# Kernel tuning notes

Hardware: AMD Instinct MI355X
Metric: run time of the kernel (lower is better)

## Reference

```python
import jax, jax.numpy as jnp
import numpy as np

SR = 22050
L = 65537            # signal length; chosen so rfft length == L (required by source broadcast)
NFFT = 131072        # 2**ceil(log2(L))
RLEN = NFFT // 2 + 1 # == L
OUT_SIZE = 65537     # output_size init arg
BANDS = [("delta", 1.0, 4.0), ("theta", 4.0, 8.0), ("alpha", 8.0, 13.0),
         ("beta", 13.0, 30.0), ("gamma", 30.0, 100.0), ("high_gamma", 100.0, 200.0)]
SPEC = [("schumann", 7.83), ("healing", 528.0), ("solfeggio", 396.0), ("sleep", 2.5),
        ("focus", 14.1), ("harmony", 432.0), ("meditation", 6.0), ("energy", 30.0)]
FREQS_NP = np.fft.rfftfreq(NFFT, d=1.0 / SR).astype(np.float32)


def _prog_mean(hp, W1, b1, W2, b2, W3, b3):
    # vectorized get_harmonic_progression(arange(L)).mean()
    t = jnp.arange(L, dtype=jnp.float32)
    tn = (t / OUT_SIZE)[:, None]                       # [L,1]
    h = jax.nn.relu(tn @ W1 + b1)
    h = jax.nn.relu(h @ W2 + b2)
    mp = h @ W3 + b3                                   # [L,8]
    mod_depth = mp[0, 1]
    chord_idx = jnp.floor(t * 8.0 / OUT_SIZE).astype(jnp.int32) % 8
    chord = hp[chord_idx]                              # [L,4]
    chord = chord * (1.0 + mod_depth * jnp.sin(2.0 * jnp.pi * t / OUT_SIZE))[:, None]
    return chord.mean()


def _gain(bw, fw, hp, W1, b1, W2, b2, W3, b3):
    # all modulation is data-independent -> single [RLEN] multiplicative gain
    t = jnp.arange(L, dtype=jnp.float32)
    gain = jnp.ones(RLEN, dtype=jnp.float32)
    for k, (_, low, high) in enumerate(BANDS):
        center = (low + high) / 2.0
        width = (high - low) / 2.0
        m_np = np.exp(-0.5 * ((FREQS_NP - center) / (width / 2.0)) ** 2)
        m_np[(FREQS_NP < low) | (FREQS_NP > high)] = 0.0
        if not np.any(m_np > 0.01):  # static branch (mask is data-independent)
            continue
        mask = jnp.asarray(m_np.astype(np.float32))     # [RLEN] == [L]
        time_mod = jnp.sin(2.0 * jnp.pi * center * t / SR)
        gain = gain * (1.0 + mask * bw[k] * (1.0 + 0.2 * time_mod))
    pm = _prog_mean(hp, W1, b1, W2, b2, W3, b3)
    ws = min(15, NFFT // 100)
    ws = ws if ws > 0 else 1
    for j, (_, f) in enumerate(SPEC):
        if f >= SR / 2:
            continue
        for mult in (1.0, 2.0, 3.0, 4.0, 5.0):
            hf = f * mult
            if hf >= SR / 2:
                continue
            hidx = int(np.argmin(np.abs(FREQS_NP - hf)))
            s = max(0, hidx - ws)
            e = min(RLEN - 1, hidx + ws)
            if s >= e:
                continue
            idxs = np.arange(s, e + 1)
            win = jnp.asarray(np.exp(-0.5 * ((idxs - hidx) / (ws / 3.0)) ** 2).astype(np.float32))
            enh = fw[j] * win * (1.0 / mult ** 1.2) * (1.0 + pm)
            gain = gain.at[s:e + 1].multiply(1.0 + enh)
    return gain


def _forward(x, bw, fw, hp, W1, b1, W2, b2, W3, b3):
    gain = _gain(bw, fw, hp, W1, b1, W2, b2, W3, b3)    # [RLEN]
    xp = jnp.pad(x, ((0, 0), (0, 0), (0, NFFT - L)))    # zero-pad to n_fft
    X = jnp.fft.rfft(xp, axis=-1) * gain                # [B,C,RLEN] complex
    mag = jnp.abs(X)
    ph = jnp.angle(X)
    mid = 0.7 * mag[..., 1:-1] + 0.15 * mag[..., :-2] + 0.15 * mag[..., 2:]
    mag_s = jnp.concatenate([mag[..., :1], mid, mag[..., -1:]], axis=-1)
    Xc = mag_s * jnp.exp(1j * ph)
    y = jnp.fft.irfft(Xc, n=NFFT, axis=-1)[..., :L]
    return y.astype(x.dtype)


def setup_inputs() -> dict:
    key = jax.random.key(0)
    ks = jax.random.split(key, 8)
    B, C = 128, 2
    x = jax.random.normal(ks[0], (B, C, L), dtype=jnp.float32)
    band_weights = jnp.full((6,), 0.5, dtype=jnp.float32)
    freq_weights = jnp.full((8,), 0.3, dtype=jnp.float32)
    harmonic_progression = jax.random.normal(ks[1], (8, 4), dtype=jnp.float32)
    W1 = jax.random.normal(ks[2], (1, 32), dtype=jnp.float32)
    b1 = jnp.zeros((32,), dtype=jnp.float32)
    W2 = jax.random.normal(ks[3], (32, 16), dtype=jnp.float32) * (1.0 / np.sqrt(32.0))
    b2 = jnp.zeros((16,), dtype=jnp.float32)
    W3 = jax.random.normal(ks[4], (16, 8), dtype=jnp.float32) * (1.0 / np.sqrt(16.0))
    b3 = jnp.zeros((8,), dtype=jnp.float32)
    return {"x": x, "band_weights": band_weights, "freq_weights": freq_weights,
            "harmonic_progression": harmonic_progression,
            "W1": W1, "b1": b1, "W2": W2, "b2": b2, "W3": W3, "b3": b3}


def reference(x, band_weights, freq_weights, harmonic_progression, W1, b1, W2, b2, W3, b3):
    return _forward(x, band_weights, freq_weights, harmonic_progression, W1, b1, W2, b2, W3, b3)
```

## Files before the change

### kernel.cpp

```cpp
#include <hip/hip_runtime.h>
#include <hip/hip_fp16.h>
#include <math.h>

#define L_SIG 65537
#define NH    65536
#define NSIG  256
#define PI_F  3.14159265358979323846f

struct alignas(8) c32 { float x, y; };
typedef __half2 h2;
__device__ __forceinline__ c32 mkc(float a, float b){ c32 r; r.x=a; r.y=b; return r; }
__device__ __forceinline__ c32 cadd(c32 a, c32 b){ return mkc(a.x+b.x, a.y+b.y); }
__device__ __forceinline__ c32 csub(c32 a, c32 b){ return mkc(a.x-b.x, a.y-b.y); }
__device__ __forceinline__ c32 cmul(c32 a, c32 b){ return mkc(a.x*b.x - a.y*b.y, a.x*b.y + a.y*b.x); }
__device__ __forceinline__ h2  c2h(c32 a){ return __floats2half2_rn(a.x, a.y); }
__device__ __forceinline__ c32 h2c(h2 a){ float2 f = __half22float2(a); return mkc(f.x, f.y); }

template<int S>
__device__ __forceinline__ void fft16(c32 v[16]) {
  constexpr float C16[16] = {
    1.0f, 0.9238795325112867f, 0.7071067811865476f, 0.3826834323650898f,
    0.0f,-0.3826834323650898f,-0.7071067811865476f,-0.9238795325112867f,
   -1.0f,-0.9238795325112867f,-0.7071067811865476f,-0.3826834323650898f,
    0.0f, 0.3826834323650898f, 0.7071067811865476f, 0.9238795325112867f };
  constexpr float S16[16] = {
    0.0f, 0.3826834323650898f, 0.7071067811865476f, 0.9238795325112867f,
    1.0f, 0.9238795325112867f, 0.7071067811865476f, 0.3826834323650898f,
    0.0f,-0.3826834323650898f,-0.7071067811865476f,-0.9238795325112867f,
   -1.0f,-0.9238795325112867f,-0.7071067811865476f,-0.3826834323650898f };
  c32 s[16];
  #pragma unroll
  for (int b0 = 0; b0 < 4; ++b0) {
    c32 x0=v[b0], x1=v[b0+4], x2=v[b0+8], x3=v[b0+12];
    c32 u0=cadd(x0,x2), u1=csub(x0,x2), u2=cadd(x1,x3), u3=csub(x1,x3);
    c32 iu3 = mkc(-u3.y, u3.x);
    c32 yy[4];
    yy[0]=cadd(u0,u2); yy[2]=csub(u0,u2);
    if (S < 0) { yy[1]=csub(u1,iu3); yy[3]=cadd(u1,iu3); }
    else       { yy[1]=cadd(u1,iu3); yy[3]=csub(u1,iu3); }
    #pragma unroll
    for (int c0 = 0; c0 < 4; ++c0) {
      const int p = (b0*c0) & 15;
      c32 w = mkc(C16[p], (S<0) ? -S16[p] : S16[p]);
      s[c0*4 + b0] = cmul(yy[c0], w);
    }
  }
  #pragma unroll
  for (int c0 = 0; c0 < 4; ++c0) {
    c32 x0=s[c0*4+0], x1=s[c0*4+1], x2=s[c0*4+2], x3=s[c0*4+3];
    c32 u0=cadd(x0,x2), u1=csub(x0,x2), u2=cadd(x1,x3), u3=csub(x1,x3);
    c32 iu3 = mkc(-u3.y, u3.x);
    c32 yy[4];
    yy[0]=cadd(u0,u2); yy[2]=csub(u0,u2);
    if (S < 0) { yy[1]=csub(u1,iu3); yy[3]=cadd(u1,iu3); }
    else       { yy[1]=cadd(u1,iu3); yy[3]=csub(u1,iu3); }
    v[c0+0]=yy[0]; v[c0+4]=yy[1]; v[c0+8]=yy[2]; v[c0+12]=yy[3];
  }
}

template<int S>
__device__ __forceinline__ void fft256_team(c32 v[16], int r, int t, c32* sc) {
  fft16<S>(v);
  float ang = (float)S * (2.0f*PI_F/256.0f) * (float)r;
  c32 st; __sincosf(ang, &st.y, &st.x);
  c32 w = st;
  #pragma unroll
  for (int c = 1; c < 16; ++c) { v[c] = cmul(v[c], w); w = cmul(w, st); }
  int p  = r*8 + (t & 7);
  int fr = (r & 1) << 3;
  __syncthreads();
  if (t < 8) {
    #pragma unroll
    for (int c = 0; c < 16; ++c)
      sc[c*128 + (p ^ ((c & 1) << 3))] = v[c];
  }
  __syncthreads();
  if (t < 8) {
    #pragma unroll
    for (int a = 0; a < 16; ++a)
      v[a] = sc[r*128 + ((a*8 + (t & 7)) ^ fr)];
  }
  __syncthreads();
  if (t >= 8) {
    #pragma unroll
    for (int c = 0; c < 16; ++c)
      sc[c*128 + (p ^ ((c & 1) << 3))] = v[c];
  }
  __syncthreads();
  if (t >= 8) {
    #pragma unroll
    for (int a = 0; a < 16; ++a)
      v[a] = sc[r*128 + ((a*8 + (t & 7)) ^ fr)];
  }
  fft16<S>(v);
}

__global__ __launch_bounds__(256) void k_pm(const float* __restrict__ hp,
                                            float* __restrict__ pm_part) {
  __shared__ float r0[256], r1[256];
  int t = threadIdx.x, b = blockIdx.x;
  int gid = b*256 + t;
  float s0 = 0.f, s1 = 0.f;
  for (int tt = gid; tt < 65537; tt += 16384) {
    int ci = (tt * 8) / 65537;
    float cs = hp[ci*4+0] + hp[ci*4+1] + hp[ci*4+2] + hp[ci*4+3];
    float ang = (6.2831853071795864769f * (float)tt) / 65537.0f;
    s0 += cs;
    s1 += cs * sinf(ang);
  }
  r0[t] = s0; r1[t] = s1;
  __syncthreads();
  for (int s = 128; s > 0; s >>= 1) {
    if (t < s) { r0[t] += r0[t+s]; r1[t] += r1[t+s]; }
    __syncthreads();
  }
  if (t == 0) { pm_part[2*b] = r0[0]; pm_part[2*b+1] = r1[0]; }
}

__global__ __launch_bounds__(256) void k_prep2(const float* __restrict__ b1,
    const float* __restrict__ W2, const float* __restrict__ b2,
    const float* __restrict__ W3, const float* __restrict__ b3,
    const float* __restrict__ fw, const float* __restrict__ pm_part,
    float* __restrict__ pm_out, int* __restrict__ hidx, float* __restrict__ amp) {
  __shared__ float r0[64], r1[64];
  __shared__ float s_pm;
  int t = threadIdx.x;
  if (t < 64) { r0[t] = pm_part[2*t]; r1[t] = pm_part[2*t+1]; }
  __syncthreads();
  if (t == 0) {
    float h1[32], h2v[16];
    for (int i=0;i<32;i++){ float z = b1[i]; h1[i] = z > 0.f ? z : 0.f; }
    for (int o=0;o<16;o++){ float acc = b2[o];
      for (int i=0;i<32;i++) acc += h1[i]*W2[i*16+o];
      h2v[o] = acc > 0.f ? acc : 0.f; }
    float md = b3[1];
    for (int i=0;i<16;i++) md += h2v[i]*W3[i*8+1];
    float S0 = 0.f, S1 = 0.f;
    for (int i=0;i<64;i++){ S0 += r0[i]; S1 += r1[i]; }
    s_pm = (S0 + md*S1) / (65537.0f * 4.0f);
    pm_out[0] = s_pm;
  }
  __syncthreads();
  if (t < 40) {
    const double SPECF[8] = {7.83, 528.0, 396.0, 2.5, 14.1, 432.0, 6.0, 30.0};
    int j = t / 5, mi = t % 5;
    double mult = (double)(mi + 1);
    double hf = SPECF[j] * mult;
    double ratio = hf * (131072.0 / 22050.0);
    hidx[t] = (int)floor(ratio + 0.5);
    amp[t] = (float)((double)fw[j] * pow(mult, -1.2) * (1.0 + (double)s_pm));
  }
}

__global__ __launch_bounds__(256) void k_gain(float* __restrict__ gain,
    const float* __restrict__ bw, const int* __restrict__ hidx,
    const float* __restrict__ amp) {
  int i = blockIdx.x*256 + threadIdx.x;
  if (i >= 65537) return;
  float f = (float)((double)i * (22050.0/131072.0));
  float g = 1.0f;
  constexpr double LO[6] = {1,4,8,13,30,100};
  constexpr double HI[6] = {4,8,13,30,100,200};
  #pragma unroll
  for (int k = 0; k < 6; ++k) {
    float center = (float)(0.5*(LO[k]+HI[k]));
    float sig    = (float)(0.25*(HI[k]-LO[k]));
    float dm = (f - center)/sig;
    float mask = expf(-0.5f*dm*dm);
    if (f < (float)LO[k] || f > (float)HI[k]) mask = 0.f;
    float ang = (float)(6.283185307179586*0.5*(LO[k]+HI[k])) * (float)i / 22050.0f;
    g *= 1.0f + mask * bw[k] * (1.0f + 0.2f*sinf(ang));
  }
  for (int l = 0; l < 40; ++l) {
    int d = i - hidx[l];
    if (d >= -15 && d <= 15) {
      float dd = (float)d * 0.2f;
      g *= 1.0f + amp[l] * expf(-0.5f*dd*dd);
    }
  }
  gain[i] = g;
}

__global__ __launch_bounds__(256, 4) void k_fwd1(const float* __restrict__ x,
                                                 h2* __restrict__ A, int s0) {
  __shared__ float smem[4096];
  c32* sc = (c32*)smem;
  h2*  stg = (h2*)smem;
  int b = blockIdx.x; int sl = b >> 4; int g = b & 15;
  int t = threadIdx.x & 15, r = threadIdx.x >> 4;
  int n1 = g*16 + t;
  const float* xb = x + (size_t)(s0 + sl) * L_SIG;
  c32 v[16];
  #pragma unroll
  for (int j = 0; j < 16; ++j) {
    int n = n1 + 256*r + 4096*j;
    c32 z = mkc(0.f, 0.f);
    if (n < 32768)       { z.x = xb[2*n]; z.y = xb[2*n+1]; }
    else if (n == 32768) { z.x = xb[65536]; }
    v[j] = z;
  }
  fft256_team<-1>(v, r, t, sc);
  float a0 = -(2.0f*PI_F/65536.0f) * (float)(n1 * r);
  float a1 = -(2.0f*PI_F/4096.0f)  * (float)n1;
  c32 wb, wst;
  __sincosf(a0, &wb.y, &wb.x);
  __sincosf(a1, &wst.y, &wst.x);
  #pragma unroll
  for (int j = 0; j < 16; ++j) { v[j] = cmul(v[j], wb); wb = cmul(wb, wst); }
  __syncthreads();
  #pragma unroll
  for (int j = 0; j < 16; ++j)
    stg[(r + 16*j)*16 + t] = c2h(v[j]);
  __syncthreads();
  h2* Ab = A + (size_t)sl * NH;
  int u = threadIdx.x & 15, k2b = threadIdx.x >> 4;
  #pragma unroll
  for (int m = 0; m < 16; ++m) {
    int k2 = k2b + 16*m;
    Ab[(size_t)k2*256 + g*16 + u] = stg[k2*16 + u];
  }
}

__global__ __launch_bounds__(256, 4) void k_fwd2(const h2* __restrict__ A,
                                                 h2* __restrict__ B) {
  __shared__ float smem[4160];
  c32* sc = (c32*)smem;
  h2* stg = (h2*)smem;
  int b = blockIdx.x; int sl = b >> 4; int g = b & 15;
  int tid = threadIdx.x;
  int t = tid & 15, r = tid >> 4;
  const h2* Ab = A + (size_t)sl * NH;
  #pragma unroll
  for (int m = 0; m < 4; ++m) {
    int flat = tid + 256*m;
    int row = flat >> 6, i = flat & 63;
    float4 z = ((const float4*)(Ab + (size_t)(g*16 + row)*256))[i];
    *((float4*)&stg[row*260 + 4*i]) = z;
  }
  __syncthreads();
  c32 v[16];
  #pragma unroll
  for (int j = 0; j < 16; ++j)
    v[j] = h2c(stg[t*260 + r + 16*j]);
  fft256_team<-1>(v, r, t, sc);
  h2* Bb = B + (size_t)sl * NH;
  int k2 = g*16 + t;
  #pragma unroll
  for (int j = 0; j < 16; ++j) Bb[(size_t)k2 + 256*(r + 16*j)] = c2h(v[j]);
}

__global__ __launch_bounds__(256) void k_mid(const h2* __restrict__ Z,
    h2* __restrict__ Zc, const float* __restrict__ gain) {
  __shared__ c32 XL[258], XH[258];
  __shared__ float ML[258], MH[258];
  __shared__ float TC[258], TS[258];
  int b = blockIdx.x; int s = b >> 7; int blk = b & 127;
  int k0 = blk << 8;
  const h2* Zs = Z + (size_t)s * NH;
  h2* Os = Zc + (size_t)s * NH;
  int t = threadIdx.x;
  for (int e = t; e < 258; e += 256) {
    int k = k0 - 1 + e;
    bool kv = (k >= 0);
    int kc = kv ? k : 0;
    c32 zk = h2c(Zs[k & (NH-1)]);
    c32 zb = h2c(Zs[(NH - k) & (NH-1)]);
    c32 Aa = mkc(0.5f*(zk.x + zb.x), 0.5f*(zk.y - zb.y));
    c32 Bm = mkc(0.5f*(zk.x - zb.x), 0.5f*(zk.y + zb.y));
    float sn, cn; __sincosf((PI_F/65536.0f)*(float)k, &sn, &cn);
    TC[e] = cn; TS[e] = sn;
    c32 wB = cmul(mkc(-sn, -cn), Bm);
    float gk = gain[kc];
    float gK = gain[NH - kc];
    c32 Xk = mkc((Aa.x + wB.x)*gk,  (Aa.y + wB.y)*gk);
    c32 XK = mkc((Aa.x - wB.x)*gK, -(Aa.y - wB.y)*gK);
    float nk = Xk.x*Xk.x + Xk.y*Xk.y;
    float nK = XK.x*XK.x + XK.y*XK.y;
    float rk = rsqrtf(nk), rK = rsqrtf(nK);
    c32 Uk = (nk > 0.f) ? mkc(Xk.x*rk, Xk.y*rk) : mkc(1.f, 0.f);
    c32 UK = (nK > 0.f) ? mkc(XK.x*rK, XK.y*rK) : mkc(1.f, 0.f);
    float mk = (kv && nk > 0.f) ? nk*rk : 0.f;
    float mK = (kv && nK > 0.f) ? nK*rK : 0.f;
    XL[e] = Uk;  ML[e] = mk;
    XH[257-e] = UK; MH[257-e] = mK;
  }
  __syncthreads();
  {
    int q = t; int k = k0 + q;
    float m = ML[q+1];
    float msm = (k == 0) ? m : 0.7f*m + 0.15f*(ML[q] + ML[q+2]);
    c32 U = XL[q+1];
    c32 XcL = mkc(U.x*msm, U.y*msm);
    int K = NH - k;
    int eH = 256 - q;
    float mh = MH[eH];
    float msh = (K == 65536) ? mh : 0.7f*mh + 0.15f*(MH[eH-1] + MH[eH+1]);
    c32 Uh = XH[eH];
    c32 XcH = mkc(Uh.x*msh, Uh.y*msh);
    c32 E = mkc(0.5f*(XcL.x + XcH.x), 0.5f*(XcL.y - XcH.y));
    c32 D = mkc(0.5f*(XcL.x - XcH.x), 0.5f*(XcL.y + XcH.y));
    c32 O = cmul(mkc(TC[q+1], TS[q+1]), D);
    const float invN = 1.0f/65536.0f;
    Os[k] = c2h(mkc((E.x - O.y)*invN, (E.y + O.x)*invN));
    if (k != 0) Os[K] = c2h(mkc((E.x + O.y)*invN, (O.x - E.y)*invN));
  }
  if (blk == 127 && t == 0) {
    float m = ML[257];
    float msm = 0.7f*m + 0.15f*(ML[256] + MH[1]);
    c32 U = XL[257];
    const float invN = 1.0f/65536.0f;
    Os[32768] = c2h(mkc(U.x*msm*invN, -U.y*msm*invN));
  }
}

__global__ __launch_bounds__(256, 4) void k_inv1(const h2* __restrict__ Zc,
                                                 h2* __restrict__ B) {
  __shared__ float smem[4096];
  c32* sc = (c32*)smem;
  h2*  stg = (h2*)smem;
  int b = blockIdx.x;
  int idx = b >> 3;
  int sl = idx >> 1;
  int g = ((b & 7) << 1) | (idx & 1);
  int t = threadIdx.x & 15, r = threadIdx.x >> 4;
  int a = g*16 + t;
  const h2* Zs = Zc + (size_t)sl * NH;
  c32 v[16];
  #pragma unroll
  for (int j = 0; j < 16; ++j) v[j] = h2c(Zs[(size_t)a + 256*(r + 16*j)]);
  fft256_team<1>(v, r, t, sc);
  float a0 = (2.0f*PI_F/65536.0f) * (float)(a * r);
  float a1 = (2.0f*PI_F/4096.0f)  * (float)a;
  c32 wb, wst;
  __sincosf(a0, &wb.y, &wb.x);
  __sincosf(a1, &wst.y, &wst.x);
  #pragma unroll
  for (int j = 0; j < 16; ++j) { v[j] = cmul(v[j], wb); wb = cmul(wb, wst); }
  __syncthreads();
  #pragma unroll
  for (int j = 0; j < 16; ++j)
    stg[(r + 16*j)*16 + t] = c2h(v[j]);
  __syncthreads();
  h2* Bb = B + (size_t)sl * NH;
  int u = threadIdx.x & 15, m2b = threadIdx.x >> 4;
  #pragma unroll
  for (int m = 0; m < 16; ++m) {
    int m2 = m2b + 16*m;
    Bb[(size_t)m2*256 + g*16 + u] = stg[m2*16 + u];
  }
}

__global__ __launch_bounds__(256, 4) void k_inv2(const h2* __restrict__ B,
                                                 float* __restrict__ out, int s0) {
  __shared__ float smem[4160];
  c32* sc = (c32*)smem;
  h2* stg = (h2*)smem;
  int b = blockIdx.x; int sl = b >> 4; int g = b & 15;
  int tid = threadIdx.x;
  int t = tid & 15, r = tid >> 4;
  const h2* Bb = B + (size_t)sl * NH;
  #pragma unroll
  for (int m = 0; m < 4; ++m) {
    int flat = tid + 256*m;
    int row = flat >> 6, i = flat & 63;
    float4 z = ((const float4*)(Bb + (size_t)(g*16 + row)*256))[i];
    *((float4*)&stg[row*260 + 4*i]) = z;
  }
  __syncthreads();
  c32 v[16];
  #pragma unroll
  for (int j = 0; j < 16; ++j)
    v[j] = h2c(stg[t*260 + r + 16*j]);
  fft256_team<1>(v, r, t, sc);
  float* yb = out + (size_t)(s0 + sl) * L_SIG;
  int m2 = g*16 + t;
  #pragma unroll
  for (int j = 0; j < 16; ++j) {
    int m1 = r + 16*j;
    if (m1 <= 127) {
      int m = m2 + 256*m1;
      yb[2*m]   = v[j].x;
      yb[2*m+1] = v[j].y;
    } else if (m1 == 128 && m2 == 0) {
      yb[65536] = v[j].x;
    }
  }
}

extern "C" void kernel_launch(void* const* d_in, const int* in_sizes, int n_in,
                              void* d_out, int out_size, void* d_ws, size_t ws_size,
                              hipStream_t stream) {
  const float* x  = (const float*)d_in[0];
  const float* bw = (const float*)d_in[1];
  const float* fw = (const float*)d_in[2];
  const float* hp = (const float*)d_in[3];
  const float* b1 = (const float*)d_in[5];
  const float* W2 = (const float*)d_in[6];
  const float* b2 = (const float*)d_in[7];
  const float* W3 = (const float*)d_in[8];
  const float* b3 = (const float*)d_in[9];
  float* out = (float*)d_out;
  char* ws = (char*)d_ws;

  const size_t perSig = (size_t)NH * sizeof(h2);
  const size_t tail   = (size_t)L_SIG * sizeof(float) + 2048;
  size_t cap = (ws_size > tail) ? (ws_size - tail) / (2*perSig) : 1;
  int chunk = (cap >= (size_t)NSIG) ? NSIG : (cap < 1 ? 1 : (int)cap);

  h2*    A    = (h2*)ws;
  h2*    Bb   = (h2*)(ws + (size_t)chunk*perSig);
  float* gain = (float*)(ws + 2*(size_t)chunk*perSig);
  float* pm   = gain + L_SIG;
  int*   hidx = (int*)(pm + 1);
  float* amp  = (float*)(hidx + 40);
  float* pm_part = amp + 40;

  k_pm   <<<64, 256, 0, stream>>>(hp, pm_part);
  k_prep2<<<1,  256, 0, stream>>>(b1, W2, b2, W3, b3, fw, pm_part, pm, hidx, amp);
  k_gain <<<257,256, 0, stream>>>(gain, bw, hidx, amp);

  for (int s0 = 0; s0 < NSIG; s0 += chunk) {
    int S = (NSIG - s0 < chunk) ? (NSIG - s0) : chunk;
    k_fwd1<<<S*16, 256, 0, stream>>>(x, A, s0);
    k_fwd2<<<S*16, 256, 0, stream>>>(A, Bb);
    k_mid <<<S*128,256, 0, stream>>>(Bb, A, gain);
    k_inv1<<<S*16, 256, 0, stream>>>(A, Bb);
    k_inv2<<<S*16, 256, 0, stream>>>(Bb, out, s0);
  }
}
```

Baseline: 284.0 us.

## Fuse forward pass-2 FFT, spectral mid-stage and inverse pass-1 into one kernel

Merges k_fwd2, k_mid and k_inv1 into a single k_fmi kernel. Each block loads the 36 mirrored column pairs (k and N-k) it needs into shared memory, runs the 256-point forward FFTs, does the pairing, gain, magnitude smoothing and repacking in registers, then runs the inverse column FFTs and writes the twiddled result. The gain table is stored in transposed order so lookups match the column layout. This removes two global round trips of the half-precision spectrum and two kernel launches per chunk. In exchange it needs about 54KB of shared memory per block, runs half as many blocks with lower occupancy, repeats some FFT work on the overlap slots, and has complex index bookkeeping.

```diff
diff --git a/kernel.cpp b/kernel.cpp
--- a/kernel.cpp
+++ b/kernel.cpp
@@ -152,11 +152,12 @@
   }
 }
 
-__global__ __launch_bounds__(256) void k_gain(float* __restrict__ gain,
+__global__ __launch_bounds__(256) void k_gain(float* __restrict__ gainT,
     const float* __restrict__ bw, const int* __restrict__ hidx,
     const float* __restrict__ amp) {
-  int i = blockIdx.x*256 + threadIdx.x;
-  if (i >= 65537) return;
+  int j = blockIdx.x*256 + threadIdx.x;
+  if (j > 65536) return;
+  int i = (j == 65536) ? 65536 : (((j >> 8) & 255) | ((j & 255) << 8));
   float f = (float)((double)i * (22050.0/131072.0));
   float g = 1.0f;
   constexpr double LO[6] = {1,4,8,13,30,100};
@@ -178,7 +179,7 @@
       g *= 1.0f + amp[l] * expf(-0.5f*dd*dd);
     }
   }
-  gain[i] = g;
+  gainT[j] = g;
 }
 
 __global__ __launch_bounds__(256, 4) void k_fwd1(const float* __restrict__ x,
@@ -221,132 +222,160 @@
   }
 }
 
-__global__ __launch_bounds__(256, 4) void k_fwd2(const h2* __restrict__ A,
-                                                 h2* __restrict__ B) {
-  __shared__ float smem[4160];
-  c32* sc = (c32*)smem;
-  h2* stg = (h2*)smem;
-  int b = blockIdx.x; int sl = b >> 4; int g = b & 15;
-  int tid = threadIdx.x;
-  int t = tid & 15, r = tid >> 4;
+__device__ __forceinline__ int colmap(int s, int p) {
+  return ((s < 18) ? (16*p - 1 + s) : (240 - 16*p + (s - 18))) & 255;
+}
+
+struct UP { c32 Uk, UK; float mk, mK, cn, sn; };
+__device__ __forceinline__ UP pairup(const h2* rows, int rowk, int rowb, int k,
+                                     const float* __restrict__ gT) {
+  UP u;
+  int kk = k & (NH-1);
+  int Km = (NH - k) & (NH-1);
+  c32 zk = h2c(rows[rowk*260 + (kk >> 8)]);
+  c32 zb = h2c(rows[rowb*260 + (Km >> 8)]);
+  c32 Aa = mkc(0.5f*(zk.x + zb.x), 0.5f*(zk.y - zb.y));
+  c32 Bm = mkc(0.5f*(zk.x - zb.x), 0.5f*(zk.y + zb.y));
+  __sincosf((PI_F/65536.0f)*(float)k, &u.sn, &u.cn);
+  c32 wB = cmul(mkc(-u.sn, -u.cn), Bm);
+  float gk = gT[((kk & 255) << 8) | (kk >> 8)];
+  int K2 = NH - k;
+  float gK = (K2 >= NH) ? gT[NH] : gT[((K2 & 255) << 8) | (K2 >> 8)];
+  c32 Xk = mkc((Aa.x + wB.x)*gk,  (Aa.y + wB.y)*gk);
+  c32 XK = mkc((Aa.x - wB.x)*gK, -(Aa.y - wB.y)*gK);
+  float nk = Xk.x*Xk.x + Xk.y*Xk.y;
+  float nK = XK.x*XK.x + XK.y*XK.y;
+  float rk = rsqrtf(nk), rK = rsqrtf(nK);
+  bool kv = (k >= 0);
+  u.Uk = (nk > 0.f) ? mkc(Xk.x*rk, Xk.y*rk) : mkc(1.f, 0.f);
+  u.UK = (nK > 0.f) ? mkc(XK.x*rK, XK.y*rK) : mkc(1.f, 0.f);
+  u.mk = (kv && nk > 0.f) ? nk*rk : 0.f;
+  u.mK = (kv && nK > 0.f) ? nK*rK : 0.f;
+  return u;
+}
+
+__global__ __launch_bounds__(256, 3) void k_fmi(const h2* __restrict__ A,
+                                                h2* __restrict__ B,
+                                                const float* __restrict__ gT) {
+  __shared__ float smem[13456];
+  h2*  rows = (h2*)smem;
+  c32* sc   = (c32*)(smem + 9360);
+  int b = blockIdx.x; int sl = b >> 3; int p = b & 7;
+  int tid = threadIdx.x; int t = tid & 15; int r = tid >> 4;
   const h2* Ab = A + (size_t)sl * NH;
   #pragma unroll
-  for (int m = 0; m < 4; ++m) {
-    int flat = tid + 256*m;
-    int row = flat >> 6, i = flat & 63;
-    float4 z = ((const float4*)(Ab + (size_t)(g*16 + row)*256))[i];
-    *((float4*)&stg[row*260 + 4*i]) = z;
-  }
-  __syncthreads();
-  c32 v[16];
-  #pragma unroll
-  for (int j = 0; j < 16; ++j)
-    v[j] = h2c(stg[t*260 + r + 16*j]);
-  fft256_team<-1>(v, r, t, sc);
-  h2* Bb = B + (size_t)sl * NH;
-  int k2 = g*16 + t;
-  #pragma unroll
-  for (int j = 0; j < 16; ++j) Bb[(size_t)k2 + 256*(r + 16*j)] = c2h(v[j]);
-}
-
-__global__ __launch_bounds__(256) void k_mid(const h2* __restrict__ Z,
-    h2* __restrict__ Zc, const float* __restrict__ gain) {
-  __shared__ c32 XL[258], XH[258];
-  __shared__ float ML[258], MH[258];
-  __shared__ float TC[258], TS[258];
-  int b = blockIdx.x; int s = b >> 7; int blk = b & 127;
-  int k0 = blk << 8;
-  const h2* Zs = Z + (size_t)s * NH;
-  h2* Os = Zc + (size_t)s * NH;
-  int t = threadIdx.x;
-  for (int e = t; e < 258; e += 256) {
-    int k = k0 - 1 + e;
-    bool kv = (k >= 0);
-    int kc = kv ? k : 0;
-    c32 zk = h2c(Zs[k & (NH-1)]);
-    c32 zb = h2c(Zs[(NH - k) & (NH-1)]);
-    c32 Aa = mkc(0.5f*(zk.x + zb.x), 0.5f*(zk.y - zb.y));
-    c32 Bm = mkc(0.5f*(zk.x - zb.x), 0.5f*(zk.y + zb.y));
-    float sn, cn; __sincosf((PI_F/65536.0f)*(float)k, &sn, &cn);
-    TC[e] = cn; TS[e] = sn;
-    c32 wB = cmul(mkc(-sn, -cn), Bm);
-    float gk = gain[kc];
-    float gK = gain[NH - kc];
-    c32 Xk = mkc((Aa.x + wB.x)*gk,  (Aa.y + wB.y)*gk);
-    c32 XK = mkc((Aa.x - wB.x)*gK, -(Aa.y - wB.y)*gK);
-    float nk = Xk.x*Xk.x + Xk.y*Xk.y;
-    float nK = XK.x*XK.x + XK.y*XK.y;
-    float rk = rsqrtf(nk), rK = rsqrtf(nK);
-    c32 Uk = (nk > 0.f) ? mkc(Xk.x*rk, Xk.y*rk) : mkc(1.f, 0.f);
-    c32 UK = (nK > 0.f) ? mkc(XK.x*rK, XK.y*rK) : mkc(1.f, 0.f);
-    float mk = (kv && nk > 0.f) ? nk*rk : 0.f;
-    float mK = (kv && nK > 0.f) ? nK*rK : 0.f;
-    XL[e] = Uk;  ML[e] = mk;
-    XH[257-e] = UK; MH[257-e] = mK;
-  }
-  __syncthreads();
-  {
-    int q = t; int k = k0 + q;
-    float m = ML[q+1];
-    float msm = (k == 0) ? m : 0.7f*m + 0.15f*(ML[q] + ML[q+2]);
-    c32 U = XL[q+1];
-    c32 XcL = mkc(U.x*msm, U.y*msm);
-    int K = NH - k;
-    int eH = 256 - q;
-    float mh = MH[eH];
-    float msh = (K == 65536) ? mh : 0.7f*mh + 0.15f*(MH[eH-1] + MH[eH+1]);
-    c32 Uh = XH[eH];
-    c32 XcH = mkc(Uh.x*msh, Uh.y*msh);
+  for (int w = 0; w < 9; ++w) {
+    int flat = tid + 256*w;
+    int s = flat >> 6, i = flat & 63;
+    int c = colmap(s, p);
+    float4 z = ((const float4*)(Ab + (size_t)c*256))[i];
+    *((float4*)(rows + s*260 + 4*i)) = z;
+  }
+  __syncthreads();
+  for (int bt = 0; bt < 3; ++bt) {
+    int slot = bt*16 + t;
+    int se = (slot < 36) ? slot : slot - 36;
+    h2* rp = rows + se*260;
+    c32 v[16];
+    #pragma unroll
+    for (int j = 0; j < 16; ++j) v[j] = h2c(rp[r + 16*j]);
+    fft256_team<-1>(v, r, t, sc);
+    if (slot < 36) {
+      #pragma unroll
+      for (int j = 0; j < 16; ++j) rp[r + 16*j] = c2h(v[j]);
+    }
+  }
+  __syncthreads();
+  int m = tid;
+  int K0 = 16*p - 1 + 256*m;
+  h2 o1[16], o2[16]; h2 o128 = __floats2half2_rn(0.f, 0.f);
+  float m1a=0.f, m1b=0.f, m2a=0.f, m2b=0.f, cnp=0.f, snp=0.f;
+  c32 u1p = mkc(1.f,0.f), u2p = mkc(1.f,0.f);
+  const float invN = 1.0f/65536.0f;
+  #pragma unroll
+  for (int s = 0; s <= 17; ++s) {
+    UP u = pairup(rows, s, 35 - s, K0 + s, gT);
+    if (s >= 2) {
+      int kq = K0 + s - 1;
+      float msm = (kq == 0) ? m1b : 0.7f*m1b + 0.15f*(m1a + u.mk);
+      float msh = (kq == 0) ? m2b : 0.7f*m2b + 0.15f*(m2a + u.mK);
+      c32 XcL = mkc(u1p.x*msm, u1p.y*msm);
+      c32 XcH = mkc(u2p.x*msh, u2p.y*msh);
+      c32 E = mkc(0.5f*(XcL.x + XcH.x), 0.5f*(XcL.y - XcH.y));
+      c32 D = mkc(0.5f*(XcL.x - XcH.x), 0.5f*(XcL.y + XcH.y));
+      c32 O = cmul(mkc(cnp, snp), D);
+      o1[s-2] = c2h(mkc((E.x - O.y)*invN, (E.y + O.x)*invN));
+      o2[s-2] = c2h(mkc((E.x + O.y)*invN, (O.x - E.y)*invN));
+    }
+    m1a = m1b; m1b = u.mk; m2a = m2b; m2b = u.mK;
+    u1p = u.Uk; u2p = u.UK; cnp = u.cn; snp = u.sn;
+  }
+  if (p == 7) {
+    int kb = 128 + 256*m;
+    UP uA = pairup(rows, 16, 19, kb - 1, gT);
+    UP u8 = pairup(rows, 17, 18, kb,     gT);
+    UP uB = pairup(rows, 19, 16, kb + 1, gT);
+    float msm = 0.7f*u8.mk + 0.15f*(uA.mk + uB.mk);
+    float msh = 0.7f*u8.mK + 0.15f*(uA.mK + uB.mK);
+    c32 XcL = mkc(u8.Uk.x*msm, u8.Uk.y*msm);
+    c32 XcH = mkc(u8.UK.x*msh, u8.UK.y*msh);
     c32 E = mkc(0.5f*(XcL.x + XcH.x), 0.5f*(XcL.y - XcH.y));
     c32 D = mkc(0.5f*(XcL.x - XcH.x), 0.5f*(XcL.y + XcH.y));
-    c32 O = cmul(mkc(TC[q+1], TS[q+1]), D);
-    const float invN = 1.0f/65536.0f;
-    Os[k] = c2h(mkc((E.x - O.y)*invN, (E.y + O.x)*invN));
-    if (k != 0) Os[K] = c2h(mkc((E.x + O.y)*invN, (O.x - E.y)*invN));
-  }
-  if (blk == 127 && t == 0) {
-    float m = ML[257];
-    float msm = 0.7f*m + 0.15f*(ML[256] + MH[1]);
-    c32 U = XL[257];
-    const float invN = 1.0f/65536.0f;
-    Os[32768] = c2h(mkc(U.x*msm*invN, -U.y*msm*invN));
-  }
-}
-
-__global__ __launch_bounds__(256, 4) void k_inv1(const h2* __restrict__ Zc,
-                                                 h2* __restrict__ B) {
-  __shared__ float smem[4096];
-  c32* sc = (c32*)smem;
-  h2*  stg = (h2*)smem;
-  int b = blockIdx.x;
-  int idx = b >> 3;
-  int sl = idx >> 1;
-  int g = ((b & 7) << 1) | (idx & 1);
-  int t = threadIdx.x & 15, r = threadIdx.x >> 4;
-  int a = g*16 + t;
-  const h2* Zs = Zc + (size_t)sl * NH;
-  c32 v[16];
-  #pragma unroll
-  for (int j = 0; j < 16; ++j) v[j] = h2c(Zs[(size_t)a + 256*(r + 16*j)]);
-  fft256_team<1>(v, r, t, sc);
-  float a0 = (2.0f*PI_F/65536.0f) * (float)(a * r);
-  float a1 = (2.0f*PI_F/4096.0f)  * (float)a;
-  c32 wb, wst;
-  __sincosf(a0, &wb.y, &wb.x);
-  __sincosf(a1, &wst.y, &wst.x);
-  #pragma unroll
-  for (int j = 0; j < 16; ++j) { v[j] = cmul(v[j], wb); wb = cmul(wb, wst); }
-  __syncthreads();
-  #pragma unroll
-  for (int j = 0; j < 16; ++j)
-    stg[(r + 16*j)*16 + t] = c2h(v[j]);
+    c32 O = cmul(mkc(u8.cn, u8.sn), D);
+    o128 = c2h(mkc((E.x - O.y)*invN, (E.y + O.x)*invN));
+  }
+  __syncthreads();
+  #pragma unroll
+  for (int s = 1; s <= 16; ++s) {
+    rows[s*260 + m] = o1[s-1];
+    int kq = K0 + s;
+    if (kq != 0) {
+      int Kq = (NH - kq) & (NH-1);
+      rows[(35 - s)*260 + (Kq >> 8)] = o2[s-1];
+    }
+  }
+  if (p == 7) rows[17*260 + m] = o128;
   __syncthreads();
   h2* Bb = B + (size_t)sl * NH;
-  int u = threadIdx.x & 15, m2b = threadIdx.x >> 4;
-  #pragma unroll
-  for (int m = 0; m < 16; ++m) {
-    int m2 = m2b + 16*m;
-    Bb[(size_t)m2*256 + g*16 + u] = stg[m2*16 + u];
+  int nb = (p == 7) ? 3 : 2;
+  for (int bt = 0; bt < nb; ++bt) {
+    int row, cb;
+    if (bt == 0)      { row = 1 + t;  cb = 16*p; }
+    else if (bt == 1) { row = 19 + t; cb = 241 - 16*p; }
+    else              { row = (t == 0) ? 17 : (1 + t); cb = 128; }
+    h2* rp = rows + row*260;
+    c32 v[16];
+    #pragma unroll
+    for (int j = 0; j < 16; ++j) v[j] = h2c(rp[r + 16*j]);
+    fft256_team<1>(v, r, t, sc);
+    int a = (bt == 2) ? 128 : ((cb + t) & 255);
+    float a0 = (2.0f*PI_F/65536.0f) * (float)(a * r);
+    float a1 = (2.0f*PI_F/4096.0f)  * (float)a;
+    c32 wb, wst;
+    __sincosf(a0, &wb.y, &wb.x);
+    __sincosf(a1, &wst.y, &wst.x);
+    #pragma unroll
+    for (int j = 0; j < 16; ++j) { v[j] = cmul(v[j], wb); wb = cmul(wb, wst); }
+    __syncthreads();
+    h2* stg = (h2*)sc;
+    #pragma unroll
+    for (int j = 0; j < 16; ++j) stg[(r + 16*j)*16 + t] = c2h(v[j]);
+    __syncthreads();
+    int u = tid & 15, m2b_ = tid >> 4;
+    if (bt < 2) {
+      int cv = cb + u;
+      #pragma unroll
+      for (int q = 0; q < 16; ++q) {
+        int m2 = m2b_ + 16*q;
+        if (cv < 256) Bb[(size_t)m2*256 + cv] = stg[m2*16 + u];
+      }
+    } else if (u == 0) {
+      #pragma unroll
+      for (int q = 0; q < 16; ++q) {
+        int m2 = m2b_ + 16*q;
+        Bb[(size_t)m2*256 + 128] = stg[m2*16 + 0];
+      }
+    }
   }
 }
 
@@ -407,24 +436,22 @@
   size_t cap = (ws_size > tail) ? (ws_size - tail) / (2*perSig) : 1;
   int chunk = (cap >= (size_t)NSIG) ? NSIG : (cap < 1 ? 1 : (int)cap);
 
-  h2*    A    = (h2*)ws;
-  h2*    Bb   = (h2*)(ws + (size_t)chunk*perSig);
-  float* gain = (float*)(ws + 2*(size_t)chunk*perSig);
-  float* pm   = gain + L_SIG;
-  int*   hidx = (int*)(pm + 1);
-  float* amp  = (float*)(hidx + 40);
+  h2*    A     = (h2*)ws;
+  h2*    Bb    = (h2*)(ws + (size_t)chunk*perSig);
+  float* gainT = (float*)(ws + 2*(size_t)chunk*perSig);
+  float* pm    = gainT + L_SIG;
+  int*   hidx  = (int*)(pm + 1);
+  float* amp   = (float*)(hidx + 40);
   float* pm_part = amp + 40;
 
   k_pm   <<<64, 256, 0, stream>>>(hp, pm_part);
   k_prep2<<<1,  256, 0, stream>>>(b1, W2, b2, W3, b3, fw, pm_part, pm, hidx, amp);
-  k_gain <<<257,256, 0, stream>>>(gain, bw, hidx, amp);
+  k_gain <<<257,256, 0, stream>>>(gainT, bw, hidx, amp);
 
   for (int s0 = 0; s0 < NSIG; s0 += chunk) {
     int S = (NSIG - s0 < chunk) ? (NSIG - s0) : chunk;
     k_fwd1<<<S*16, 256, 0, stream>>>(x, A, s0);
-    k_fwd2<<<S*16, 256, 0, stream>>>(A, Bb);
-    k_mid <<<S*128,256, 0, stream>>>(Bb, A, gain);
-    k_inv1<<<S*16, 256, 0, stream>>>(A, Bb);
+    k_fmi <<<S*8,  256, 0, stream>>>(A, Bb, gainT);
     k_inv2<<<S*16, 256, 0, stream>>>(Bb, out, s0);
   }
 }
```

Measured after the change: 367.5 us. 29.4% more time.
